# Optimization experiments

Hardware: AMD Instinct MI355X
Metric: run time of the kernel (lower is better)

The kernel has to match this reference:

```python
import jax, jax.numpy as jnp
import numpy as np
import math

NB_STEPS = 50  # matches init kwarg nb_steps


def cc_quadrature(nb_steps):
    # Clenshaw-Curtis weights/nodes, identical to UMNN's compute_cc_weights.
    lam = np.arange(nb_steps + 1, dtype=np.float64).reshape(-1, 1)
    lam = np.cos((lam @ lam.T) * math.pi / nb_steps)
    lam[:, 0] = 0.5
    lam[:, -1] = 0.5 * lam[:, -1]
    lam = lam * 2.0 / nb_steps
    W = np.arange(nb_steps + 1, dtype=np.float64).reshape(-1, 1)
    W[np.arange(1, nb_steps + 1, 2)] = 0
    W = 2.0 / (1.0 - W ** 2)
    W[0] = 1
    W[np.arange(1, nb_steps + 1, 2)] = 0
    cc_weights = (lam.T @ W).astype(np.float32)                 # [K, 1]
    steps = np.cos(np.arange(nb_steps + 1, dtype=np.float64).reshape(-1, 1)
                   * math.pi / nb_steps).astype(np.float32)     # [K, 1]
    return jnp.asarray(cc_weights), jnp.asarray(steps)


def integrand_mlp(xh, W1, b1, W2, b2, W3, b3, W4, b4):
    y = jax.nn.relu(jnp.einsum('bkd,hd->bkh', xh, W1) + b1)
    y = jax.nn.relu(jnp.einsum('bkh,gh->bkg', y, W2) + b2)
    y = jax.nn.relu(jnp.einsum('bkg,fg->bkf', y, W3) + b3)
    y = jnp.einsum('bkf,of->bko', y, W4) + b4
    return jax.nn.elu(y) + 1.0


def setup_inputs() -> dict:
    key = jax.random.key(0)
    ks = jax.random.split(key, 10)
    B, HD, IN_D = 16384, 128, 64
    x = jax.random.normal(ks[0], (B, 1), dtype=jnp.float32)
    h = jax.random.normal(ks[1], (B, IN_D - 1), dtype=jnp.float32)
    def lin(k, fan_out, fan_in):
        return jax.random.normal(k, (fan_out, fan_in), dtype=jnp.float32) / np.sqrt(fan_in)
    return {
        'x': x, 'h': h,
        'W1': lin(ks[2], HD, IN_D), 'b1': jax.random.normal(ks[3], (HD,), dtype=jnp.float32) * 0.01,
        'W2': lin(ks[4], HD, HD),   'b2': jax.random.normal(ks[5], (HD,), dtype=jnp.float32) * 0.01,
        'W3': lin(ks[6], HD, HD),   'b3': jax.random.normal(ks[7], (HD,), dtype=jnp.float32) * 0.01,
        'W4': lin(ks[8], 1, HD),    'b4': jax.random.normal(ks[9], (1,), dtype=jnp.float32) * 0.01,
    }


def reference(x, h, W1, b1, W2, b2, W3, b3, W4, b4):
    cc_w, steps = cc_quadrature(NB_STEPS)          # [K,1], [K,1]
    xmax = jnp.max(x) + 10.0
    x0 = x                                          # [B,1]
    xT = jnp.zeros_like(x) + xmax                   # xfinal broadcast
    # quadrature points X_steps: [B, K, 1]
    X = x0[:, None, :] + (xT - x0)[:, None, :] * (steps[None, :, :] + 1.0) * 0.5
    B, K = X.shape[0], X.shape[1]
    hK = jnp.broadcast_to(h[:, None, :], (B, K, h.shape[1]))
    xh = jnp.concatenate([X, hK], axis=-1)          # [B, K, in_d]
    f = integrand_mlp(xh, W1, b1, W2, b2, W3, b3, W4, b4)  # [B, K, 1]
    z = jnp.sum(f * cc_w[None, :, :], axis=1)       # [B, 1]
    return z * (xT - x0) * 0.5
```

## Files before the change

kernel.cpp:

```cpp
#include <hip/hip_runtime.h>
#include <hip/hip_bf16.h>
#include <math.h>


#define B_N    16384
#define KQ     51
#define HD     128
#define IND    64
#define BLK    128
#define RPB    16
#define GRID   (B_N / RPB)
#define TPB    ((RPB * KQ) / 16)

typedef __attribute__((ext_vector_type(8))) short short8;
typedef __attribute__((ext_vector_type(4))) float f32x4;

union S8U { short8 s8; unsigned u[4]; };

__device__ __forceinline__ unsigned short f2bf(float f) {
    __hip_bfloat16 t = __float2bfloat16(f);
    return *reinterpret_cast<unsigned short*>(&t);
}

#if defined(__gfx950__) && defined(__has_builtin)
#if __has_builtin(__builtin_amdgcn_cvt_pk_bf16_f32)
#define HAVE_PK_BF16 1
#endif
#endif

__device__ __forceinline__ unsigned pk_bf16(float lo, float hi) {
#ifdef HAVE_PK_BF16
    typedef __attribute__((ext_vector_type(2))) __bf16 bfv2;
    bfv2 r = __builtin_amdgcn_cvt_pk_bf16_f32(lo, hi);
    return *reinterpret_cast<unsigned*>(&r);
#else
    return (unsigned)f2bf(lo) | ((unsigned)f2bf(hi) << 16);
#endif
}

__launch_bounds__(BLK, 2)
__global__ void umnn_fused(const float* __restrict__ x,  const float* __restrict__ h,
                           const float* __restrict__ W1, const float* __restrict__ b1,
                           const float* __restrict__ W2, const float* __restrict__ b2,
                           const float* __restrict__ W3, const float* __restrict__ b3,
                           const float* __restrict__ W4, const float* __restrict__ b4,
                           float* __restrict__ out)
{
    __shared__ __align__(16) float hpL[RPB * HD];
    __shared__ __align__(16) char  y2x[2][4096];
    __shared__ __align__(16) float hshT[63 * 20];
    __shared__ __align__(16) float vs4[TPB * 64];
    __shared__ __align__(16) float b2f[HD], b3f[HD];
    __shared__ float xL[RPB];
    __shared__ float sSteps[KQ], sCcw[KQ];
    __shared__ float red2[2];

    const int tid  = threadIdx.x;
    const int w    = tid >> 6;
    const int lane = tid & 63;
    const int q    = lane >> 4;
    const int lm   = lane & 15;
    const int swz  = lm & 7;
    const int rowBase = blockIdx.x * RPB;

    if (tid < KQ) {
        const int j = tid;
        const float pi50 = 0.06283185307179586f;
        sSteps[j] = __cosf((float)j * pi50);
        float s = 0.0f;
        for (int i = 0; i <= 50; i += 2) {
            float Wi = (i == 0) ? 1.0f : 2.0f / (1.0f - (float)(i * i));
            float lam;
            if (j == 0) lam = 0.5f;
            else {
                int mp = (i * j) % 100;
                lam = __cosf((float)mp * pi50);
                if (j == 50) lam *= 0.5f;
            }
            s += (lam * 0.04f) * Wi;
        }
        sCcw[j] = s;
    }
    if (tid < HD) {
        b2f[tid] = b2[tid];
        b3f[tid] = b3[tid];
    }
    {
        const f32x4* x4 = (const f32x4*)x;
        float mx = -1e30f;
        for (int i = tid; i < B_N / 4; i += BLK) {
            f32x4 v = x4[i];
            mx = fmaxf(fmaxf(mx, fmaxf(v[0], v[1])), fmaxf(v[2], v[3]));
        }
        #pragma unroll
        for (int d = 32; d > 0; d >>= 1) mx = fmaxf(mx, __shfl_xor(mx, d));
        if (lane == 0) red2[w] = mx;
    }
    for (int i = tid; i < RPB * 63; i += BLK) {
        int r = i / 63, d = i - r * 63;
        hshT[d * 20 + r] = h[rowBase * 63 + i];
    }
    if (tid < RPB) xL[tid] = x[rowBase + tid];
    __syncthreads();

    const float xmax = fmaxf(red2[0], red2[1]) + 10.0f;

    {
        const int n = tid;
        float acc[RPB];
        const float b1v = b1[n];
        #pragma unroll
        for (int r = 0; r < RPB; ++r) acc[r] = b1v;

        auto doFMA = [&](float wv, int d) {
            const float* ht = hshT + d * 20;
            #pragma unroll
            for (int rc = 0; rc < RPB / 4; ++rc) {
                f32x4 hv = *(const f32x4*)(ht + rc * 4);
                acc[rc * 4 + 0] = fmaf(wv, hv[0], acc[rc * 4 + 0]);
                acc[rc * 4 + 1] = fmaf(wv, hv[1], acc[rc * 4 + 1]);
                acc[rc * 4 + 2] = fmaf(wv, hv[2], acc[rc * 4 + 2]);
                acc[rc * 4 + 3] = fmaf(wv, hv[3], acc[rc * 4 + 3]);
            }
        };

        const float* w1row = W1 + n * IND;
        f32x4 wc = *(const f32x4*)(w1row);
        f32x4 wn = *(const f32x4*)(w1row + 4);
        doFMA(wc[1], 0); doFMA(wc[2], 1); doFMA(wc[3], 2);
        int d = 3;
        #pragma unroll 1
        for (int j = 1; j < IND / 4; ++j) {
            wc = wn;
            if (j + 1 < IND / 4)
                wn = *(const f32x4*)(w1row + 4 * (j + 1));
            doFMA(wc[0], d); doFMA(wc[1], d + 1);
            doFMA(wc[2], d + 2); doFMA(wc[3], d + 3);
            d += 4;
        }
        #pragma unroll
        for (int r = 0; r < RPB; ++r) hpL[r * HD + n] = acc[r];
    }
    __syncthreads();

    const int bIoff = q * 16;

    if (w == 0) {
        __builtin_amdgcn_s_setprio(0);
        float w1x[32];
        #pragma unroll
        for (int kk = 0; kk < 4; ++kk)
            #pragma unroll
            for (int j = 0; j < 8; ++j)
                w1x[kk * 8 + j] = W1[(kk * 32 + q * 8 + j) * IND];

        short8 W2A[8][4];
        #pragma unroll
        for (int nt = 0; nt < 8; ++nt) {
            #pragma unroll
            for (int kk = 0; kk < 4; ++kk) {
                const float* p2 = W2 + (nt * 16 + lm) * HD + kk * 32 + q * 8;
                f32x4 v0 = *(const f32x4*)(p2);
                f32x4 v1 = *(const f32x4*)(p2 + 4);
                S8U a2;
                a2.u[0] = pk_bf16(v0[0], v0[1]);
                a2.u[1] = pk_bf16(v0[2], v0[3]);
                a2.u[2] = pk_bf16(v1[0], v1[1]);
                a2.u[3] = pk_bf16(v1[2], v1[3]);
                W2A[nt][kk] = a2.s8;
            }
        }
        int wrOff[8];
        #pragma unroll
        for (int nt = 0; nt < 8; ++nt)
            wrOff[nt] = lm * 256 + (((2 * nt + (q >> 1)) ^ swz) << 4) + ((q & 1) << 3);
        const char* b2c = (const char*)b2f;

        #pragma unroll 1
        for (int tt = 0; tt < TPB; ++tt) {
            const int s    = tt * 16 + lm;
            const unsigned row = (unsigned)s / KQ;
            const int k    = s - (int)row * KQ;
            const float x0 = xL[row];
            const float X  = fmaf((xmax - x0) * 0.5f, sSteps[k] + 1.0f, x0);
            short8 Y1[4];
            #pragma unroll
            for (int kk = 0; kk < 4; ++kk) {
                const float* hp = hpL + row * HD + kk * 32 + q * 8;
                f32x4 ha = *(const f32x4*)hp;
                f32x4 hb = *(const f32x4*)(hp + 4);
                S8U u;
                u.u[0] = pk_bf16(fmaxf(fmaf(X, w1x[kk*8+0], ha[0]), 0.f),
                                 fmaxf(fmaf(X, w1x[kk*8+1], ha[1]), 0.f));
                u.u[1] = pk_bf16(fmaxf(fmaf(X, w1x[kk*8+2], ha[2]), 0.f),
                                 fmaxf(fmaf(X, w1x[kk*8+3], ha[3]), 0.f));
                u.u[2] = pk_bf16(fmaxf(fmaf(X, w1x[kk*8+4], hb[0]), 0.f),
                                 fmaxf(fmaf(X, w1x[kk*8+5], hb[1]), 0.f));
                u.u[3] = pk_bf16(fmaxf(fmaf(X, w1x[kk*8+6], hb[2]), 0.f),
                                 fmaxf(fmaf(X, w1x[kk*8+7], hb[3]), 0.f));
                Y1[kk] = u.s8;
            }

            f32x4 C[8];
            #pragma unroll
            for (int nt = 0; nt < 8; ++nt)
                C[nt] = *(const f32x4*)(b2c + nt * 64 + bIoff);
            #pragma unroll
            for (int kk = 0; kk < 4; ++kk)
                #pragma unroll
                for (int nt = 0; nt < 8; ++nt)
                    C[nt] = __builtin_amdgcn_mfma_f32_16x16x32_bf16(W2A[nt][kk], Y1[kk], C[nt], 0, 0, 0);

            char* d2 = y2x[tt & 1];
            #pragma unroll
            for (int nt = 0; nt < 8; ++nt) {
                unsigned lo = pk_bf16(fmaxf(C[nt][0], 0.f), fmaxf(C[nt][1], 0.f));
                unsigned hi = pk_bf16(fmaxf(C[nt][2], 0.f), fmaxf(C[nt][3], 0.f));
                *(int2*)(d2 + wrOff[nt]) = make_int2((int)lo, (int)hi);
            }
            __syncthreads();
        }
    } else {
        __builtin_amdgcn_s_setprio(1);
        short8 W3A[8][4];
        f32x4  W4c[8];
        #pragma unroll
        for (int nt = 0; nt < 8; ++nt) {
            #pragma unroll
            for (int kk = 0; kk < 4; ++kk) {
                const float* p3 = W3 + (nt * 16 + lm) * HD + kk * 32 + q * 8;
                f32x4 v0 = *(const f32x4*)(p3);
                f32x4 v1 = *(const f32x4*)(p3 + 4);
                S8U a3;
                a3.u[0] = pk_bf16(v0[0], v0[1]);
                a3.u[1] = pk_bf16(v0[2], v0[3]);
                a3.u[2] = pk_bf16(v1[0], v1[1]);
                a3.u[3] = pk_bf16(v1[2], v1[3]);
                W3A[nt][kk] = a3.s8;
            }
            W4c[nt] = *(const f32x4*)(W4 + nt * 16 + q * 4);
        }
        const float b4v = b4[0];
        int rdOff[4];
        #pragma unroll
        for (int kk = 0; kk < 4; ++kk)
            rdOff[kk] = lm * 256 + (((kk * 4 + q) ^ swz) << 4);
        const char* b3c = (const char*)b3f;

        #pragma unroll 1
        for (int tt = 0; tt < TPB; ++tt) {
            __syncthreads();
            const char* s2 = y2x[tt & 1];

            short8 Y2[4];
            #pragma unroll
            for (int kk = 0; kk < 4; ++kk)
                Y2[kk] = *(const short8*)(s2 + rdOff[kk]);
            f32x4 C[8];
            #pragma unroll
            for (int nt = 0; nt < 8; ++nt)
                C[nt] = *(const f32x4*)(b3c + nt * 64 + bIoff);

            #pragma unroll
            for (int kk = 0; kk < 4; ++kk)
                #pragma unroll
                for (int nt = 0; nt < 8; ++nt)
                    C[nt] = __builtin_amdgcn_mfma_f32_16x16x32_bf16(W3A[nt][kk], Y2[kk], C[nt], 0, 0, 0);

            float p = 0.f;
            #pragma unroll
            for (int nt = 0; nt < 8; ++nt) {
                p = fmaf(fmaxf(C[nt][0], 0.f), W4c[nt][0], p);
                p = fmaf(fmaxf(C[nt][1], 0.f), W4c[nt][1], p);
                p = fmaf(fmaxf(C[nt][2], 0.f), W4c[nt][2], p);
                p = fmaf(fmaxf(C[nt][3], 0.f), W4c[nt][3], p);
            }
            vs4[tt * 64 + lane] = p;
        }

        {
            const int r   = lane >> 2;
            const int sub = lane & 3;
            float a = 0.f;
            #pragma unroll 1
            for (int j = 0; j < 13; ++j) {
                int k = sub + 4 * j;
                if (k < KQ) {
                    int s   = r * KQ + k;
                    int tt  = s >> 4;
                    int lm2 = s & 15;
                    const float* vb = vs4 + tt * 64 + lm2;
                    float y4 = vb[0] + vb[16] + vb[32] + vb[48] + b4v;
                    float f  = (y4 > 0.f) ? (y4 + 1.f) : __expf(y4);
                    a = fmaf(f, sCcw[k], a);
                }
            }
            a += __shfl_xor(a, 1);
            a += __shfl_xor(a, 2);
            if (sub == 0)
                out[rowBase + r] = a * (xmax - xL[r]) * 0.5f;
        }
    }
}

extern "C" void kernel_launch(void* const* d_in, const int* in_sizes, int n_in,
                              void* d_out, int out_size, void* d_ws, size_t ws_size,
                              hipStream_t stream)
{
    const float* x  = (const float*)d_in[0];
    const float* h  = (const float*)d_in[1];
    const float* W1 = (const float*)d_in[2];
    const float* b1 = (const float*)d_in[3];
    const float* W2 = (const float*)d_in[4];
    const float* b2 = (const float*)d_in[5];
    const float* W3 = (const float*)d_in[6];
    const float* b3 = (const float*)d_in[7];
    const float* W4 = (const float*)d_in[8];
    const float* b4 = (const float*)d_in[9];
    float* out = (float*)d_out;

    umnn_fused<<<GRID, BLK, 0, stream>>>(x, h, W1, b1, W2, b2, W3, b3,
                                         W4, b4, out);
}
```

Baseline: 162.3 us.

## Split layer-2/3 MFMA work across both waves instead of producer/consumer wave roles

Replaces the wave-specialized pipeline (wave 0 runs layer 1+2, wave 1 runs layer 3+4) with a symmetric split where each wave owns half the output tiles of both layers. Each wave builds half of Y1 into a new double-buffered LDS tile, and the loop is software-pipelined so layer-3 work for tile t-1 overlaps layer-2 work for tile t. This aims to balance MFMA load across the two waves and halve the per-wave weight register footprint. In exchange it adds an extra LDS round trip for Y1, a cross-wave shuffle and partial-sum reduction for the W4 dot product, and reuses the hshT LDS region for the output partials.

```diff
diff --git a/kernel.cpp b/kernel.cpp
--- a/kernel.cpp
+++ b/kernel.cpp
@@ -47,13 +47,15 @@
                            float* __restrict__ out)
 {
     __shared__ __align__(16) float hpL[RPB * HD];
+    __shared__ __align__(16) char  y1x[2][4096];
     __shared__ __align__(16) char  y2x[2][4096];
-    __shared__ __align__(16) float hshT[63 * 20];
-    __shared__ __align__(16) float vs4[TPB * 64];
+    __shared__ __align__(16) float poolF[2 * TPB * 32];
     __shared__ __align__(16) float b2f[HD], b3f[HD];
     __shared__ float xL[RPB];
     __shared__ float sSteps[KQ], sCcw[KQ];
     __shared__ float red2[2];
+
+    float* hshT = poolF;
 
     const int tid  = threadIdx.x;
     const int w    = tid >> 6;
@@ -61,6 +63,7 @@
     const int q    = lane >> 4;
     const int lm   = lane & 15;
     const int swz  = lm & 7;
+    const int ntB  = w * 4;
     const int rowBase = blockIdx.x * RPB;
 
     if (tid < KQ) {
@@ -143,163 +146,218 @@
     }
     __syncthreads();
 
-    const int bIoff = q * 16;
+    float w1x[16];
+    #pragma unroll
+    for (int kh = 0; kh < 2; ++kh)
+        #pragma unroll
+        for (int j = 0; j < 8; ++j)
+            w1x[kh * 8 + j] = W1[((2 * w + kh) * 32 + q * 8 + j) * IND];
+
+    short8 W2A[4][4], W3A[4][4];
+    #pragma unroll
+    for (int nt = 0; nt < 4; ++nt) {
+        #pragma unroll
+        for (int kk = 0; kk < 4; ++kk) {
+            const float* p2 = W2 + ((ntB + nt) * 16 + lm) * HD + kk * 32 + q * 8;
+            f32x4 a0 = *(const f32x4*)(p2);
+            f32x4 a1 = *(const f32x4*)(p2 + 4);
+            S8U u2;
+            u2.u[0] = pk_bf16(a0[0], a0[1]);
+            u2.u[1] = pk_bf16(a0[2], a0[3]);
+            u2.u[2] = pk_bf16(a1[0], a1[1]);
+            u2.u[3] = pk_bf16(a1[2], a1[3]);
+            W2A[nt][kk] = u2.s8;
+            const float* p3 = W3 + ((ntB + nt) * 16 + lm) * HD + kk * 32 + q * 8;
+            f32x4 c0 = *(const f32x4*)(p3);
+            f32x4 c1 = *(const f32x4*)(p3 + 4);
+            S8U u3;
+            u3.u[0] = pk_bf16(c0[0], c0[1]);
+            u3.u[1] = pk_bf16(c0[2], c0[3]);
+            u3.u[2] = pk_bf16(c1[0], c1[1]);
+            u3.u[3] = pk_bf16(c1[2], c1[3]);
+            W3A[nt][kk] = u3.s8;
+        }
+    }
+    f32x4 W4c[4];
+    #pragma unroll
+    for (int nt = 0; nt < 4; ++nt)
+        W4c[nt] = *(const f32x4*)(W4 + (ntB + nt) * 16 + q * 4);
+    const float b4v = b4[0];
+
+    int rdOff[4];
+    #pragma unroll
+    for (int kk = 0; kk < 4; ++kk)
+        rdOff[kk] = lm * 256 + (((kk * 4 + q) ^ swz) << 4);
+    int bld[2];
+    #pragma unroll
+    for (int kh = 0; kh < 2; ++kh)
+        bld[kh] = lm * 256 + ((((2 * w + kh) * 4 + q) ^ swz) << 4);
+    int wrOff[4];
+    #pragma unroll
+    for (int nt = 0; nt < 4; ++nt)
+        wrOff[nt] = lm * 256 + (((2 * (ntB + nt) + (q >> 1)) ^ swz) << 4)
+                  + ((q & 1) << 3);
+    const int bI = ntB * 64 + q * 16;
+    const char* b2c = (const char*)b2f;
+    const char* b3c = (const char*)b3f;
+    float* vsW = poolF + w * (TPB * 32);
+
+    auto buildY1 = [&](int ib, char* dst) {
+        const int s   = ib * 16 + lm;
+        const unsigned row = (unsigned)s / KQ;
+        const int k   = s - (int)row * KQ;
+        const float x0 = xL[row];
+        const float X  = fmaf((xmax - x0) * 0.5f, sSteps[k] + 1.0f, x0);
+        #pragma unroll
+        for (int kh = 0; kh < 2; ++kh) {
+            const int kk = 2 * w + kh;
+            const float* hp = hpL + row * HD + kk * 32 + q * 8;
+            f32x4 ha = *(const f32x4*)hp;
+            f32x4 hb = *(const f32x4*)(hp + 4);
+            S8U u;
+            u.u[0] = pk_bf16(fmaxf(fmaf(X, w1x[kh*8+0], ha[0]), 0.f),
+                             fmaxf(fmaf(X, w1x[kh*8+1], ha[1]), 0.f));
+            u.u[1] = pk_bf16(fmaxf(fmaf(X, w1x[kh*8+2], ha[2]), 0.f),
+                             fmaxf(fmaf(X, w1x[kh*8+3], ha[3]), 0.f));
+            u.u[2] = pk_bf16(fmaxf(fmaf(X, w1x[kh*8+4], hb[0]), 0.f),
+                             fmaxf(fmaf(X, w1x[kh*8+5], hb[1]), 0.f));
+            u.u[3] = pk_bf16(fmaxf(fmaf(X, w1x[kh*8+6], hb[2]), 0.f),
+                             fmaxf(fmaf(X, w1x[kh*8+7], hb[3]), 0.f));
+            *(short8*)(dst + bld[kh]) = u.s8;
+        }
+    };
+
+    buildY1(0, y1x[0]);
+    __syncthreads();
+
+    {
+        short8 Y1f[4];
+        #pragma unroll
+        for (int kk = 0; kk < 4; ++kk)
+            Y1f[kk] = *(const short8*)(y1x[0] + rdOff[kk]);
+        buildY1(1, y1x[1]);
+        f32x4 C[4];
+        #pragma unroll
+        for (int nt = 0; nt < 4; ++nt)
+            C[nt] = *(const f32x4*)(b2c + nt * 64 + bI);
+        #pragma unroll
+        for (int kk = 0; kk < 4; ++kk)
+            #pragma unroll
+            for (int nt = 0; nt < 4; ++nt)
+                C[nt] = __builtin_amdgcn_mfma_f32_16x16x32_bf16(W2A[nt][kk], Y1f[kk], C[nt], 0, 0, 0);
+        #pragma unroll
+        for (int nt = 0; nt < 4; ++nt) {
+            unsigned lo = pk_bf16(fmaxf(C[nt][0], 0.f), fmaxf(C[nt][1], 0.f));
+            unsigned hi = pk_bf16(fmaxf(C[nt][2], 0.f), fmaxf(C[nt][3], 0.f));
+            *(int2*)(y2x[0] + wrOff[nt]) = make_int2((int)lo, (int)hi);
+        }
+        __syncthreads();
+    }
+
+    #pragma unroll 1
+    for (int t = 1; t < TPB; ++t) {
+        const char* s1 = y1x[t & 1];
+        const char* s2 = y2x[(t - 1) & 1];
+        short8 Y1f[4], Y2f[4];
+        #pragma unroll
+        for (int kk = 0; kk < 4; ++kk)
+            Y2f[kk] = *(const short8*)(s2 + rdOff[kk]);
+        #pragma unroll
+        for (int kk = 0; kk < 4; ++kk)
+            Y1f[kk] = *(const short8*)(s1 + rdOff[kk]);
+
+        f32x4 C[4];
+        #pragma unroll
+        for (int nt = 0; nt < 4; ++nt)
+            C[nt] = *(const f32x4*)(b3c + nt * 64 + bI);
+        #pragma unroll
+        for (int kk = 0; kk < 4; ++kk)
+            #pragma unroll
+            for (int nt = 0; nt < 4; ++nt)
+                C[nt] = __builtin_amdgcn_mfma_f32_16x16x32_bf16(W3A[nt][kk], Y2f[kk], C[nt], 0, 0, 0);
+        float p = 0.f;
+        #pragma unroll
+        for (int nt = 0; nt < 4; ++nt) {
+            p = fmaf(fmaxf(C[nt][0], 0.f), W4c[nt][0], p);
+            p = fmaf(fmaxf(C[nt][1], 0.f), W4c[nt][1], p);
+            p = fmaf(fmaxf(C[nt][2], 0.f), W4c[nt][2], p);
+            p = fmaf(fmaxf(C[nt][3], 0.f), W4c[nt][3], p);
+        }
+        p += __shfl_xor(p, 32);
+        if (lane < 32) vsW[(t - 1) * 32 + lane] = p;
+
+        if (t + 1 < TPB) buildY1(t + 1, y1x[(t + 1) & 1]);
+
+        f32x4 D[4];
+        #pragma unroll
+        for (int nt = 0; nt < 4; ++nt)
+            D[nt] = *(const f32x4*)(b2c + nt * 64 + bI);
+        #pragma unroll
+        for (int kk = 0; kk < 4; ++kk)
+            #pragma unroll
+            for (int nt = 0; nt < 4; ++nt)
+                D[nt] = __builtin_amdgcn_mfma_f32_16x16x32_bf16(W2A[nt][kk], Y1f[kk], D[nt], 0, 0, 0);
+        char* d2 = y2x[t & 1];
+        #pragma unroll
+        for (int nt = 0; nt < 4; ++nt) {
+            unsigned lo = pk_bf16(fmaxf(D[nt][0], 0.f), fmaxf(D[nt][1], 0.f));
+            unsigned hi = pk_bf16(fmaxf(D[nt][2], 0.f), fmaxf(D[nt][3], 0.f));
+            *(int2*)(d2 + wrOff[nt]) = make_int2((int)lo, (int)hi);
+        }
+        __syncthreads();
+    }
+
+    {
+        const char* s2 = y2x[(TPB - 1) & 1];
+        short8 Y2f[4];
+        #pragma unroll
+        for (int kk = 0; kk < 4; ++kk)
+            Y2f[kk] = *(const short8*)(s2 + rdOff[kk]);
+        f32x4 C[4];
+        #pragma unroll
+        for (int nt = 0; nt < 4; ++nt)
+            C[nt] = *(const f32x4*)(b3c + nt * 64 + bI);
+        #pragma unroll
+        for (int kk = 0; kk < 4; ++kk)
+            #pragma unroll
+            for (int nt = 0; nt < 4; ++nt)
+                C[nt] = __builtin_amdgcn_mfma_f32_16x16x32_bf16(W3A[nt][kk], Y2f[kk], C[nt], 0, 0, 0);
+        float p = 0.f;
+        #pragma unroll
+        for (int nt = 0; nt < 4; ++nt) {
+            p = fmaf(fmaxf(C[nt][0], 0.f), W4c[nt][0], p);
+            p = fmaf(fmaxf(C[nt][1], 0.f), W4c[nt][1], p);
+            p = fmaf(fmaxf(C[nt][2], 0.f), W4c[nt][2], p);
+            p = fmaf(fmaxf(C[nt][3], 0.f), W4c[nt][3], p);
+        }
+        p += __shfl_xor(p, 32);
+        if (lane < 32) vsW[(TPB - 1) * 32 + lane] = p;
+        __syncthreads();
+    }
 
     if (w == 0) {
-        __builtin_amdgcn_s_setprio(0);
-        float w1x[32];
-        #pragma unroll
-        for (int kk = 0; kk < 4; ++kk)
-            #pragma unroll
-            for (int j = 0; j < 8; ++j)
-                w1x[kk * 8 + j] = W1[(kk * 32 + q * 8 + j) * IND];
-
-        short8 W2A[8][4];
-        #pragma unroll
-        for (int nt = 0; nt < 8; ++nt) {
-            #pragma unroll
-            for (int kk = 0; kk < 4; ++kk) {
-                const float* p2 = W2 + (nt * 16 + lm) * HD + kk * 32 + q * 8;
-                f32x4 v0 = *(const f32x4*)(p2);
-                f32x4 v1 = *(const f32x4*)(p2 + 4);
-                S8U a2;
-                a2.u[0] = pk_bf16(v0[0], v0[1]);
-                a2.u[1] = pk_bf16(v0[2], v0[3]);
-                a2.u[2] = pk_bf16(v1[0], v1[1]);
-                a2.u[3] = pk_bf16(v1[2], v1[3]);
-                W2A[nt][kk] = a2.s8;
+        const float* v0 = poolF;
+        const float* v1 = poolF + TPB * 32;
+        const int r   = lane >> 2;
+        const int sub = lane & 3;
+        float a = 0.f;
+        #pragma unroll 1
+        for (int j = 0; j < 13; ++j) {
+            int k = sub + 4 * j;
+            if (k < KQ) {
+                int s   = r * KQ + k;
+                int tt  = s >> 4;
+                int lm2 = s & 15;
+                float y4 = v0[tt * 32 + lm2] + v0[tt * 32 + 16 + lm2]
+                         + v1[tt * 32 + lm2] + v1[tt * 32 + 16 + lm2] + b4v;
+                float f  = (y4 > 0.f) ? (y4 + 1.f) : __expf(y4);
+                a = fmaf(f, sCcw[k], a);
             }
         }
-        int wrOff[8];
-        #pragma unroll
-        for (int nt = 0; nt < 8; ++nt)
-            wrOff[nt] = lm * 256 + (((2 * nt + (q >> 1)) ^ swz) << 4) + ((q & 1) << 3);
-        const char* b2c = (const char*)b2f;
-
-        #pragma unroll 1
-        for (int tt = 0; tt < TPB; ++tt) {
-            const int s    = tt * 16 + lm;
-            const unsigned row = (unsigned)s / KQ;
-            const int k    = s - (int)row * KQ;
-            const float x0 = xL[row];
-            const float X  = fmaf((xmax - x0) * 0.5f, sSteps[k] + 1.0f, x0);
-            short8 Y1[4];
-            #pragma unroll
-            for (int kk = 0; kk < 4; ++kk) {
-                const float* hp = hpL + row * HD + kk * 32 + q * 8;
-                f32x4 ha = *(const f32x4*)hp;
-                f32x4 hb = *(const f32x4*)(hp + 4);
-                S8U u;
-                u.u[0] = pk_bf16(fmaxf(fmaf(X, w1x[kk*8+0], ha[0]), 0.f),
-                                 fmaxf(fmaf(X, w1x[kk*8+1], ha[1]), 0.f));
-                u.u[1] = pk_bf16(fmaxf(fmaf(X, w1x[kk*8+2], ha[2]), 0.f),
-                                 fmaxf(fmaf(X, w1x[kk*8+3], ha[3]), 0.f));
-                u.u[2] = pk_bf16(fmaxf(fmaf(X, w1x[kk*8+4], hb[0]), 0.f),
-                                 fmaxf(fmaf(X, w1x[kk*8+5], hb[1]), 0.f));
-                u.u[3] = pk_bf16(fmaxf(fmaf(X, w1x[kk*8+6], hb[2]), 0.f),
-                                 fmaxf(fmaf(X, w1x[kk*8+7], hb[3]), 0.f));
-                Y1[kk] = u.s8;
-            }
-
-            f32x4 C[8];
-            #pragma unroll
-            for (int nt = 0; nt < 8; ++nt)
-                C[nt] = *(const f32x4*)(b2c + nt * 64 + bIoff);
-            #pragma unroll
-            for (int kk = 0; kk < 4; ++kk)
-                #pragma unroll
-                for (int nt = 0; nt < 8; ++nt)
-                    C[nt] = __builtin_amdgcn_mfma_f32_16x16x32_bf16(W2A[nt][kk], Y1[kk], C[nt], 0, 0, 0);
-
-            char* d2 = y2x[tt & 1];
-            #pragma unroll
-            for (int nt = 0; nt < 8; ++nt) {
-                unsigned lo = pk_bf16(fmaxf(C[nt][0], 0.f), fmaxf(C[nt][1], 0.f));
-                unsigned hi = pk_bf16(fmaxf(C[nt][2], 0.f), fmaxf(C[nt][3], 0.f));
-                *(int2*)(d2 + wrOff[nt]) = make_int2((int)lo, (int)hi);
-            }
-            __syncthreads();
-        }
-    } else {
-        __builtin_amdgcn_s_setprio(1);
-        short8 W3A[8][4];
-        f32x4  W4c[8];
-        #pragma unroll
-        for (int nt = 0; nt < 8; ++nt) {
-            #pragma unroll
-            for (int kk = 0; kk < 4; ++kk) {
-                const float* p3 = W3 + (nt * 16 + lm) * HD + kk * 32 + q * 8;
-                f32x4 v0 = *(const f32x4*)(p3);
-                f32x4 v1 = *(const f32x4*)(p3 + 4);
-                S8U a3;
-                a3.u[0] = pk_bf16(v0[0], v0[1]);
-                a3.u[1] = pk_bf16(v0[2], v0[3]);
-                a3.u[2] = pk_bf16(v1[0], v1[1]);
-                a3.u[3] = pk_bf16(v1[2], v1[3]);
-                W3A[nt][kk] = a3.s8;
-            }
-            W4c[nt] = *(const f32x4*)(W4 + nt * 16 + q * 4);
-        }
-        const float b4v = b4[0];
-        int rdOff[4];
-        #pragma unroll
-        for (int kk = 0; kk < 4; ++kk)
-            rdOff[kk] = lm * 256 + (((kk * 4 + q) ^ swz) << 4);
-        const char* b3c = (const char*)b3f;
-
-        #pragma unroll 1
-        for (int tt = 0; tt < TPB; ++tt) {
-            __syncthreads();
-            const char* s2 = y2x[tt & 1];
-
-            short8 Y2[4];
-            #pragma unroll
-            for (int kk = 0; kk < 4; ++kk)
-                Y2[kk] = *(const short8*)(s2 + rdOff[kk]);
-            f32x4 C[8];
-            #pragma unroll
-            for (int nt = 0; nt < 8; ++nt)
-                C[nt] = *(const f32x4*)(b3c + nt * 64 + bIoff);
-
-            #pragma unroll
-            for (int kk = 0; kk < 4; ++kk)
-                #pragma unroll
-                for (int nt = 0; nt < 8; ++nt)
-                    C[nt] = __builtin_amdgcn_mfma_f32_16x16x32_bf16(W3A[nt][kk], Y2[kk], C[nt], 0, 0, 0);
-
-            float p = 0.f;
-            #pragma unroll
-            for (int nt = 0; nt < 8; ++nt) {
-                p = fmaf(fmaxf(C[nt][0], 0.f), W4c[nt][0], p);
-                p = fmaf(fmaxf(C[nt][1], 0.f), W4c[nt][1], p);
-                p = fmaf(fmaxf(C[nt][2], 0.f), W4c[nt][2], p);
-                p = fmaf(fmaxf(C[nt][3], 0.f), W4c[nt][3], p);
-            }
-            vs4[tt * 64 + lane] = p;
-        }
-
-        {
-            const int r   = lane >> 2;
-            const int sub = lane & 3;
-            float a = 0.f;
-            #pragma unroll 1
-            for (int j = 0; j < 13; ++j) {
-                int k = sub + 4 * j;
-                if (k < KQ) {
-                    int s   = r * KQ + k;
-                    int tt  = s >> 4;
-                    int lm2 = s & 15;
-                    const float* vb = vs4 + tt * 64 + lm2;
-                    float y4 = vb[0] + vb[16] + vb[32] + vb[48] + b4v;
-                    float f  = (y4 > 0.f) ? (y4 + 1.f) : __expf(y4);
-                    a = fmaf(f, sCcw[k], a);
-                }
-            }
-            a += __shfl_xor(a, 1);
-            a += __shfl_xor(a, 2);
-            if (sub == 0)
-                out[rowBase + r] = a * (xmax - xL[r]) * 0.5f;
-        }
+        a += __shfl_xor(a, 1);
+        a += __shfl_xor(a, 2);
+        if (sub == 0)
+            out[rowBase + r] = a * (xmax - xL[r]) * 0.5f;
     }
 }
 
```

Result: slower. 168.6 us (+3.9%).
